# Optimization experiments

Hardware: AMD Instinct MI355X
Metric: run time of the kernel (lower is better)

Reference implementation:

```python
import jax, jax.numpy as jnp
import numpy as np

N = 20000
E = 640000
H, C = 4, 64
L = 3
B = 16
EPS = 1e-5


def setup_inputs() -> dict:
    key = jax.random.key(0)
    ks = jax.random.split(key, 12)
    x = jax.random.normal(ks[0], (N, 256), dtype=jnp.float32)
    edge_index = jax.random.randint(ks[1], (2, E), 0, N, dtype=jnp.int64)
    batch = jnp.sort(jax.random.randint(ks[2], (N,), 0, B, dtype=jnp.int64))
    s = 0.05
    return {
        "x": x,
        "edge_index": edge_index,
        "batch": batch,
        "Wl": jax.random.normal(ks[3], (L, 256, H * C), dtype=jnp.float32) * s,
        "bl": jnp.zeros((L, H * C), dtype=jnp.float32),
        "Wr": jax.random.normal(ks[4], (L, 256, H * C), dtype=jnp.float32) * s,
        "br": jnp.zeros((L, H * C), dtype=jnp.float32),
        "att": jax.random.normal(ks[5], (L, H, C), dtype=jnp.float32) * s,
        "conv_bias": jnp.zeros((L, H * C), dtype=jnp.float32),
        "prelu_a": jnp.full((L,), 0.25, dtype=jnp.float32),
        "norm_w": jnp.ones((H * C,), dtype=jnp.float32),
        "norm_b": jnp.zeros((H * C,), dtype=jnp.float32),
        "norm_alpha": jnp.ones((H * C,), dtype=jnp.float32),
        "fc_W": jax.random.normal(ks[6], (H * C, 128), dtype=jnp.float32) * s,
        "fc_b": jnp.zeros((128,), dtype=jnp.float32),
    }


def graph_norm(h, w, b, alpha):
    # GraphNorm with batch=None: all rows form one segment (as in source forward)
    mean = jnp.mean(h, axis=0, keepdims=True)
    shifted = h - alpha * mean
    var = jnp.mean(shifted * shifted, axis=0, keepdims=True)
    return w * shifted / jnp.sqrt(var + EPS) + b


def gatv2_layer(h, src, dst, Wl, bl, Wr, br, att, bias):
    xl = (h @ Wl + bl).reshape(N, H, C)  # source transform
    xr = (h @ Wr + br).reshape(N, H, C)  # target transform
    m = jax.nn.leaky_relu(xl[src] + xr[dst], negative_slope=0.2)  # [Etot,H,C]
    e = jnp.einsum("ehc,hc->eh", m, att)  # [Etot,H]
    emax = jax.ops.segment_max(e, dst, num_segments=N)  # self-loops guarantee coverage
    ex = jnp.exp(e - emax[dst])
    denom = jax.ops.segment_sum(ex, dst, num_segments=N)
    alpha = ex / denom[dst]
    out = jax.ops.segment_sum(alpha[:, :, None] * xl[src], dst, num_segments=N)
    return out.reshape(N, H * C) + bias


def reference(x, edge_index, batch, Wl, bl, Wr, br, att, conv_bias, prelu_a,
              norm_w, norm_b, norm_alpha, fc_W, fc_b):
    loop = jnp.arange(N, dtype=edge_index.dtype)
    src = jnp.concatenate([edge_index[0], loop])  # add self-loops (PyG default)
    dst = jnp.concatenate([edge_index[1], loop])
    h = x
    for l in range(L):
        h = gatv2_layer(h, src, dst, Wl[l], bl[l], Wr[l], br[l], att[l], conv_bias[l])
        h = graph_norm(h, norm_w, norm_b, norm_alpha)
        h = jnp.where(h >= 0, h, prelu_a[l] * h)  # PReLU; dropout is identity in eval
    pooled = jax.ops.segment_sum(h, batch, num_segments=B)  # global_add_pool
    pooled = graph_norm(pooled, norm_w, norm_b, norm_alpha)  # shared norm reused after pool
    return pooled @ fc_W + fc_b
```

## Files before the change

kernel.cpp:

```cpp
#include <hip/hip_runtime.h>
#include <math.h>

#define N_NODES 20000
#define N_EDGES 640000
#define ETOT (N_EDGES + N_NODES)
#define HC 256
#define NLAYER 3
#define NBATCH 16
#define GEPS 1e-5f
#define NSLOT 64

typedef unsigned short u16;
typedef unsigned int u32;
typedef __attribute__((ext_vector_type(8))) short short8;
typedef __attribute__((ext_vector_type(4))) float floatx4;

__device__ __forceinline__ u16 f2bf(float f) {
    u32 u = __float_as_uint(f);
    u32 r = (u + 0x7FFFu + ((u >> 16) & 1u)) >> 16;
    return (u16)r;
}

__device__ __forceinline__ float4 bf2f4(uint2 u) {
    float4 r;
    r.x = __uint_as_float(u.x << 16);
    r.y = __uint_as_float(u.x & 0xFFFF0000u);
    r.z = __uint_as_float(u.y << 16);
    r.w = __uint_as_float(u.y & 0xFFFF0000u);
    return r;
}

__device__ __forceinline__ float dpp_red16(float x) {
    x += __int_as_float(__builtin_amdgcn_update_dpp(0, __float_as_int(x), 0xB1, 0xF, 0xF, true));
    x += __int_as_float(__builtin_amdgcn_update_dpp(0, __float_as_int(x), 0x4E, 0xF, 0xF, true));
    x += __int_as_float(__builtin_amdgcn_update_dpp(0, __float_as_int(x), 0x141, 0xF, 0xF, true));
    x += __int_as_float(__builtin_amdgcn_update_dpp(0, __float_as_int(x), 0x140, 0xF, 0xF, true));
    return x;
}


__global__ __launch_bounds__(256) void prep(const float* __restrict__ x, u16* __restrict__ xbf,
                                            const float* __restrict__ Wl, const float* __restrict__ Wr,
                                            u16* __restrict__ WT, uint4* __restrict__ zbase, int zq) {
    int b = blockIdx.x, tid = threadIdx.x;
    if (b < 1000) {
        for (int i = b * 256 + tid; i < 640000; i += 256000) {
            const float4* x4 = (const float4*)x + (size_t)i * 2;
            float4 a = x4[0], c = x4[1];
            u16 o[8] = {f2bf(a.x), f2bf(a.y), f2bf(a.z), f2bf(a.w),
                        f2bf(c.x), f2bf(c.y), f2bf(c.z), f2bf(c.w)};
            ((uint4*)xbf)[i] = *(const uint4*)o;
        }
    } else if (b < 1384) {
        __shared__ float T[32][33];
        int bi = b - 1000;
        int kb = bi & 7, nbk = (bi >> 3) & 15, l = bi >> 7;
        int n0 = nbk * 32, k0 = kb * 32;
        const float* W = ((n0 < 256) ? Wl : Wr) + (size_t)l * 65536;
        int nn = n0 & 255;
        int tx = tid & 31, ty = tid >> 5;
        #pragma unroll
        for (int i = 0; i < 4; ++i)
            T[ty + i * 8][tx] = W[(size_t)(k0 + ty + i * 8) * 256 + nn + tx];
        __syncthreads();
        u16* outw = WT + (size_t)l * 512 * 256;
        #pragma unroll
        for (int i = 0; i < 4; ++i)
            outw[(size_t)(n0 + ty + i * 8) * 256 + k0 + tx] = f2bf(T[tx][ty + i * 8]);
    } else {
        uint4 z = make_uint4(0, 0, 0, 0);
        for (int i = (b - 1384) * 256 + tid; i < zq; i += 120 * 256) zbase[i] = z;
    }
}


__global__ void count_deg(const int* __restrict__ dst, int* __restrict__ deg) {
    int e = blockIdx.x * 256 + threadIdx.x;
    if (e < N_EDGES) atomicAdd(&deg[dst[e]], 1);
}

__global__ __launch_bounds__(1024) void scan_excl(int* __restrict__ data, int* __restrict__ cursor) {
    __shared__ int wsum[16];
    __shared__ int carry_s;
    int tid = threadIdx.x, lane = tid & 63, wid = tid >> 6;
    if (tid == 0) carry_s = 0;
    __syncthreads();
    for (int base = 0; base < N_NODES; base += 1024) {
        int i = base + tid;
        int v = (i < N_NODES) ? (data[i] + 1) : 0;
        int x = v;
        #pragma unroll
        for (int off = 1; off < 64; off <<= 1) {
            int t = __shfl_up(x, off);
            if (lane >= off) x += t;
        }
        if (lane == 63) wsum[wid] = x;
        __syncthreads();
        int carry = carry_s;
        __syncthreads();
        if (tid == 0) {
            int run = 0;
            #pragma unroll
            for (int w2 = 0; w2 < 16; ++w2) { int t = wsum[w2]; wsum[w2] = run; run += t; }
            carry_s = carry + run;
        }
        __syncthreads();
        int excl = carry + wsum[wid] + x - v;
        if (i < N_NODES) { data[i] = excl; cursor[i] = excl; }
        __syncthreads();
    }
    if (tid == 0) data[N_NODES] = carry_s;
}

__global__ void scatter_edges(const int* __restrict__ src, const int* __restrict__ dst,
                              int* __restrict__ cursor, int* __restrict__ col) {
    int t = blockIdx.x * 256 + threadIdx.x;
    if (t < N_NODES) {
        int p = atomicAdd(&cursor[t], 1);
        col[p] = t;
    } else if (t < N_NODES + N_EDGES) {
        int e = t - N_NODES;
        int p = atomicAdd(&cursor[dst[e]], 1);
        col[p] = src[e];
    }
}


__global__ __launch_bounds__(256) void gemm_mfma(
    const u16* __restrict__ Asrc, const float* __restrict__ slots_prev,
    const float* __restrict__ nw, const float* __restrict__ nb, const float* __restrict__ na,
    const float* __restrict__ pa, int prelu_idx, int use_norm,
    const u16* __restrict__ WT,
    const float* __restrict__ b0, const float* __restrict__ b1,
    u16* __restrict__ xlb, u16* __restrict__ xrb) {
    __shared__ u16 As[128][40];
    __shared__ u16 Bs[128][40];
    __shared__ float wcL[256], bbL[256];
    int row0 = blockIdx.x * 128;
    int nstrip = blockIdx.y;
    int ncol0 = nstrip * 128;
    const float* bias = (nstrip < 2) ? b0 : b1;
    u16* outp = (nstrip < 2) ? xlb : xrb;
    int c0 = (nstrip & 1) * 128;

    int tid = threadIdx.x;
    float ap = 0.f;
    if (use_norm) {
        int c = tid;
        float sum = 0.f, sq = 0.f;
        for (int s = 0; s < NSLOT; ++s) {
            sum += slots_prev[s * 512 + c];
            sq += slots_prev[s * 512 + 256 + c];
        }
        const float invn = 1.f / (float)N_NODES;
        float mean = sum * invn, Eh2 = sq * invn;
        float a = na[c];
        float var = Eh2 - (2.f * a - a * a) * mean * mean;
        float wc = nw[c] * rsqrtf(var + GEPS);
        wcL[c] = wc;
        bbL[c] = nb[c] - a * mean * wc;
        ap = pa[prelu_idx];
        __syncthreads();
    }

    int wave = tid >> 6, lane = tid & 63;
    int wm = (wave & 1) * 64, wn = (wave >> 1) * 64;
    int quad = lane >> 4, l16 = lane & 15;

    floatx4 acc[4][4] = {};

    int sr = tid >> 1;
    int sh = (tid & 1) * 16;

    for (int k0 = 0; k0 < 256; k0 += 32) {
        int gr = row0 + sr;
        uint4 av0 = make_uint4(0, 0, 0, 0), av1 = make_uint4(0, 0, 0, 0);
        if (gr < N_NODES) {
            const u16* p = Asrc + (size_t)gr * 256 + k0 + sh;
            av0 = *(const uint4*)p;
            av1 = *(const uint4*)(p + 8);
        }
        if (use_norm) {
            int kb2 = k0 + sh;
            u16 tmp[16];
            *(uint4*)tmp = av0;
            *(uint4*)(tmp + 8) = av1;
            u16 outv[16];
            #pragma unroll
            for (int j = 0; j < 16; ++j) {
                float vv = __uint_as_float(((u32)tmp[j]) << 16);
                float t2 = vv * wcL[kb2 + j] + bbL[kb2 + j];
                t2 = fmaxf(t2, ap * t2);
                outv[j] = f2bf(t2);
            }
            av0 = *(const uint4*)outv;
            av1 = *(const uint4*)(outv + 8);
        }
        const u16* q = WT + (size_t)(ncol0 + sr) * 256 + k0 + sh;
        uint4 bw0 = *(const uint4*)q;
        uint4 bw1 = *(const uint4*)(q + 8);
        *(uint4*)&As[sr][sh] = av0;
        *(uint4*)&As[sr][sh + 8] = av1;
        *(uint4*)&Bs[sr][sh] = bw0;
        *(uint4*)&Bs[sr][sh + 8] = bw1;
        __syncthreads();

        short8 af[4], bfr[4];
        #pragma unroll
        for (int mi = 0; mi < 4; ++mi)
            af[mi] = *(const short8*)&As[wm + mi * 16 + l16][quad * 8];
        #pragma unroll
        for (int ni = 0; ni < 4; ++ni)
            bfr[ni] = *(const short8*)&Bs[wn + ni * 16 + l16][quad * 8];
        #pragma unroll
        for (int mi = 0; mi < 4; ++mi)
            #pragma unroll
            for (int ni = 0; ni < 4; ++ni)
                acc[mi][ni] = __builtin_amdgcn_mfma_f32_16x16x32_bf16(af[mi], bfr[ni], acc[mi][ni], 0, 0, 0);
        __syncthreads();
    }

    #pragma unroll
    for (int ni = 0; ni < 4; ++ni) {
        int col = c0 + wn + ni * 16 + l16;
        float bv = bias[col];
        #pragma unroll
        for (int mi = 0; mi < 4; ++mi) {
            int gr = row0 + wm + mi * 16 + quad * 4;
            #pragma unroll
            for (int r = 0; r < 4; ++r) {
                if (gr + r < N_NODES)
                    outp[(size_t)(gr + r) * 256 + col] = f2bf(acc[mi][ni][r] + bv);
            }
        }
    }
}


__global__ __launch_bounds__(1024) void gat_agg(
    const u16* __restrict__ xlb, const u16* __restrict__ xrb,
    const int* __restrict__ rowptr, const int* __restrict__ col,
    const float* __restrict__ att_l, const float* __restrict__ bias_l,
    u16* __restrict__ hB, float* __restrict__ slot) {
    __shared__ float sred[16][520];
    int wid = threadIdx.x >> 6, lane = threadIdx.x & 63;
    int node = blockIdx.x * 16 + wid;
    const uint2* xl2 = (const uint2*)xlb;
    float4 attv = ((const float4*)att_l)[lane];
    float4 xrv = bf2f4(((const uint2*)xrb)[(size_t)node * 64 + lane]);
    int beg = rowptr[node], end = rowptr[node + 1];

    float denom = 0.f;
    float4 acc = make_float4(0.f, 0.f, 0.f, 0.f);

    int j = beg;
    for (; j + 8 <= end; j += 8) {
        int s[8];
        uint2 raw[8];
        float4 a[8];
        float p[8];
        #pragma unroll
        for (int u = 0; u < 8; ++u) s[u] = col[j + u];
        #pragma unroll
        for (int u = 0; u < 8; ++u) raw[u] = xl2[(size_t)s[u] * 64 + lane];
        #pragma unroll
        for (int u = 0; u < 8; ++u) {
            a[u] = bf2f4(raw[u]);
            float vx = a[u].x + xrv.x, vy = a[u].y + xrv.y;
            float vz = a[u].z + xrv.z, vw = a[u].w + xrv.w;
            vx = fmaxf(vx, 0.2f * vx);
            vy = fmaxf(vy, 0.2f * vy);
            vz = fmaxf(vz, 0.2f * vz);
            vw = fmaxf(vw, 0.2f * vw);
            p[u] = vx * attv.x + vy * attv.y + vz * attv.z + vw * attv.w;
        }
        #pragma unroll
        for (int u = 0; u < 8; ++u) p[u] = dpp_red16(p[u]);
        #pragma unroll
        for (int u = 0; u < 8; ++u) {
            float w = __expf(p[u]);
            denom += w;
            acc.x += w * a[u].x; acc.y += w * a[u].y;
            acc.z += w * a[u].z; acc.w += w * a[u].w;
        }
    }
    for (; j < end; ++j) {
        int s = col[j];
        float4 a = bf2f4(xl2[(size_t)s * 64 + lane]);
        float vx = a.x + xrv.x, vy = a.y + xrv.y;
        float vz = a.z + xrv.z, vw = a.w + xrv.w;
        vx = fmaxf(vx, 0.2f * vx);
        vy = fmaxf(vy, 0.2f * vy);
        vz = fmaxf(vz, 0.2f * vz);
        vw = fmaxf(vw, 0.2f * vw);
        float p = vx * attv.x + vy * attv.y + vz * attv.z + vw * attv.w;
        p = dpp_red16(p);
        float w = __expf(p);
        denom += w;
        acc.x += w * a.x; acc.y += w * a.y; acc.z += w * a.z; acc.w += w * a.w;
    }

    float inv = 1.f / denom;
    float4 b4 = ((const float4*)bias_l)[lane];
    float4 o;
    o.x = acc.x * inv + b4.x; o.y = acc.y * inv + b4.y;
    o.z = acc.z * inv + b4.z; o.w = acc.w * inv + b4.w;
    u16 ob[4] = {f2bf(o.x), f2bf(o.y), f2bf(o.z), f2bf(o.w)};
    ((uint2*)hB)[(size_t)node * 64 + lane] = *(const uint2*)ob;

    int cb2 = lane * 4;
    sred[wid][cb2 + 0] = o.x; sred[wid][cb2 + 1] = o.y;
    sred[wid][cb2 + 2] = o.z; sred[wid][cb2 + 3] = o.w;
    sred[wid][256 + cb2 + 0] = o.x * o.x; sred[wid][256 + cb2 + 1] = o.y * o.y;
    sred[wid][256 + cb2 + 2] = o.z * o.z; sred[wid][256 + cb2 + 3] = o.w * o.w;
    __syncthreads();
    int t = threadIdx.x;
    if (t < 512) {
        float s = 0.f;
        #pragma unroll
        for (int w = 0; w < 16; ++w) s += sred[w][t];
        atomicAdd(&slot[(blockIdx.x & (NSLOT - 1)) * 512 + t], s);
    }
}


__global__ __launch_bounds__(256) void pool_kernel(const u16* __restrict__ hB,
                                                   const int* __restrict__ batch,
                                                   const float* __restrict__ slots2,
                                                   const float* __restrict__ nw, const float* __restrict__ nb,
                                                   const float* __restrict__ na, const float* __restrict__ pa,
                                                   float* __restrict__ pooled) {
    __shared__ float accs[NBATCH][256];
    int c = threadIdx.x;
    float sum = 0.f, sq = 0.f;
    for (int s = 0; s < NSLOT; ++s) {
        sum += slots2[s * 512 + c];
        sq += slots2[s * 512 + 256 + c];
    }
    const float invn = 1.f / (float)N_NODES;
    float mean = sum * invn, Eh2 = sq * invn;
    float a = na[c];
    float var = Eh2 - (2.f * a - a * a) * mean * mean;
    float wc = nw[c] * rsqrtf(var + GEPS);
    float bb = nb[c] - a * mean * wc;
    float ap = pa[2];

    #pragma unroll
    for (int b = 0; b < NBATCH; ++b) accs[b][c] = 0.f;
    int r0 = blockIdx.x * 100;
    int r1 = min(N_NODES, r0 + 100);
    for (int i = r0; i < r1; ++i) {
        float v = __uint_as_float(((u32)hB[(size_t)i * 256 + c]) << 16);
        v = v * wc + bb;
        v = fmaxf(v, ap * v);
        accs[batch[i]][c] += v;
    }
    int bmin = batch[r0], bmax = batch[r1 - 1];
    for (int b = bmin; b <= bmax; ++b) atomicAdd(&pooled[b * 256 + c], accs[b][c]);
}


__global__ __launch_bounds__(256) void poolnorm_fc(const float* __restrict__ pooled,
                                                   const float* __restrict__ nw, const float* __restrict__ nb,
                                                   const float* __restrict__ na,
                                                   const float* __restrict__ fcW, const float* __restrict__ fcb,
                                                   float* __restrict__ out) {
    __shared__ float pn[NBATCH][256];
    int c = threadIdx.x;
    float mean = 0.f, sq = 0.f;
    #pragma unroll
    for (int i = 0; i < NBATCH; ++i) {
        float v = pooled[i * 256 + c];
        mean += v; sq += v * v;
    }
    mean *= (1.f / NBATCH); sq *= (1.f / NBATCH);
    float a = na[c];
    float var = sq - (2.f * a - a * a) * mean * mean;
    float wc = nw[c] * rsqrtf(var + GEPS);
    float bb = nb[c] - a * mean * wc;
    #pragma unroll
    for (int i = 0; i < NBATCH; ++i)
        pn[i][c] = pooled[i * 256 + c] * wc + bb;
    __syncthreads();
    int o = c & 127, bset = c >> 7;
    for (int b = bset; b < NBATCH; b += 2) {
        float s = fcb[o];
        for (int k = 0; k < 256; ++k) s += pn[b][k] * fcW[k * 128 + o];
        out[b * 128 + o] = s;
    }
}


extern "C" void kernel_launch(void* const* d_in, const int* in_sizes, int n_in,
                              void* d_out, int out_size, void* d_ws, size_t ws_size,
                              hipStream_t stream) {
    const float* x    = (const float*)d_in[0];
    const int*   ei   = (const int*)d_in[1];
    const int*   batch= (const int*)d_in[2];
    const float* Wl   = (const float*)d_in[3];
    const float* bl   = (const float*)d_in[4];
    const float* Wr   = (const float*)d_in[5];
    const float* br   = (const float*)d_in[6];
    const float* att  = (const float*)d_in[7];
    const float* cb   = (const float*)d_in[8];
    const float* pa   = (const float*)d_in[9];
    const float* nw   = (const float*)d_in[10];
    const float* nb   = (const float*)d_in[11];
    const float* na   = (const float*)d_in[12];
    const float* fcW  = (const float*)d_in[13];
    const float* fcb  = (const float*)d_in[14];
    float* out = (float*)d_out;

    char* ws = (char*)d_ws;
    size_t off = 0;
    auto carve = [&](size_t bytes) -> void* {
        void* p = (void*)(ws + off);
        off += (bytes + 255) & ~(size_t)255;
        return p;
    };
    size_t z0 = off;
    int*   rowptr = (int*)carve((N_NODES + 1) * sizeof(int));
    float* slots  = (float*)carve((size_t)NLAYER * NSLOT * 512 * sizeof(float));
    float* pooled = (float*)carve(NBATCH * HC * sizeof(float));
    size_t z1 = off;
    int*   cursor = (int*)carve(N_NODES * sizeof(int));
    int*   colidx = (int*)carve((size_t)ETOT * sizeof(int));
    u16*   xlb    = (u16*)carve((size_t)N_NODES * HC * sizeof(u16));
    u16*   xrb    = (u16*)carve((size_t)N_NODES * HC * sizeof(u16));
    u16*   hB     = (u16*)carve((size_t)N_NODES * HC * sizeof(u16));
    u16*   xbf    = (u16*)carve((size_t)N_NODES * HC * sizeof(u16));
    u16*   WT     = (u16*)carve((size_t)NLAYER * 512 * 256 * sizeof(u16));

    int zq = (int)((z1 - z0) / 16);
    const int* srcp = ei;
    const int* dstp = ei + N_EDGES;

    prep<<<1504, 256, 0, stream>>>(x, xbf, Wl, Wr, WT, (uint4*)(ws + z0), zq);
    count_deg<<<(N_EDGES + 255) / 256, 256, 0, stream>>>(dstp, rowptr);
    scan_excl<<<1, 1024, 0, stream>>>(rowptr, cursor);
    scatter_edges<<<(ETOT + 255) / 256, 256, 0, stream>>>(srcp, dstp, cursor, colidx);

    for (int l = 0; l < NLAYER; ++l) {
        const u16* Asrc = (l == 0) ? xbf : hB;
        const float* slots_prev = slots + (size_t)((l > 0) ? (l - 1) : 0) * NSLOT * 512;
        gemm_mfma<<<dim3(157, 4), 256, 0, stream>>>(Asrc, slots_prev, nw, nb, na, pa,
                                                    (l > 0) ? (l - 1) : 0, (l > 0) ? 1 : 0,
                                                    WT + (size_t)l * 512 * 256,
                                                    bl + l * 256, br + l * 256, xlb, xrb);
        gat_agg<<<1250, 1024, 0, stream>>>(xlb, xrb, rowptr, colidx, att + l * 256, cb + l * 256,
                                           hB, slots + (size_t)l * NSLOT * 512);
    }
    pool_kernel<<<200, 256, 0, stream>>>(hB, batch, slots + (size_t)2 * NSLOT * 512,
                                         nw, nb, na, pa, pooled);
    poolnorm_fc<<<1, 256, 0, stream>>>(pooled, nw, nb, na, fcW, fcb, out);
}
```

Before: 533.8 us.

## Parallelize scan, shrink aggregation blocks, vectorize norm loads, split final FC

The degree scan now runs in one pass: each of 1024 threads handles 20 contiguous nodes, replacing the 20-iteration loop with repeated barriers. The aggregation kernel moves from 1024-thread to 256-thread blocks, four nodes per block, which gives finer scheduling but four times as many atomic adds into the stats slots. The norm weights in the GEMM prologue are loaded as float4 vectors. The single-block pool-norm and FC step is split into a norm kernel and a 16-block FC kernel, which adds one launch but spreads the FC work across more compute units.

```diff
diff --git a/kernel.cpp b/kernel.cpp
--- a/kernel.cpp
+++ b/kernel.cpp
@@ -81,35 +81,39 @@
 
 __global__ __launch_bounds__(1024) void scan_excl(int* __restrict__ data, int* __restrict__ cursor) {
     __shared__ int wsum[16];
-    __shared__ int carry_s;
-    int tid = threadIdx.x, lane = tid & 63, wid = tid >> 6;
-    if (tid == 0) carry_s = 0;
+    int t = threadIdx.x, lane = t & 63, wid = t >> 6;
+    int i0 = t * 20;
+    int d[20];
+    int tot = 0;
+    #pragma unroll
+    for (int j = 0; j < 20; ++j) {
+        int i = i0 + j;
+        int v = (i < N_NODES) ? (data[i] + 1) : 0;
+        d[j] = v;
+        tot += v;
+    }
+    int x = tot;
+    #pragma unroll
+    for (int off = 1; off < 64; off <<= 1) {
+        int tmp = __shfl_up(x, off);
+        if (lane >= off) x += tmp;
+    }
+    if (lane == 63) wsum[wid] = x;
     __syncthreads();
-    for (int base = 0; base < N_NODES; base += 1024) {
-        int i = base + tid;
-        int v = (i < N_NODES) ? (data[i] + 1) : 0;
-        int x = v;
-        #pragma unroll
-        for (int off = 1; off < 64; off <<= 1) {
-            int t = __shfl_up(x, off);
-            if (lane >= off) x += t;
-        }
-        if (lane == 63) wsum[wid] = x;
-        __syncthreads();
-        int carry = carry_s;
-        __syncthreads();
-        if (tid == 0) {
-            int run = 0;
-            #pragma unroll
-            for (int w2 = 0; w2 < 16; ++w2) { int t = wsum[w2]; wsum[w2] = run; run += t; }
-            carry_s = carry + run;
-        }
-        __syncthreads();
-        int excl = carry + wsum[wid] + x - v;
-        if (i < N_NODES) { data[i] = excl; cursor[i] = excl; }
-        __syncthreads();
-    }
-    if (tid == 0) data[N_NODES] = carry_s;
+    if (t == 0) {
+        int run = 0;
+        #pragma unroll
+        for (int w = 0; w < 16; ++w) { int tv = wsum[w]; wsum[w] = run; run += tv; }
+    }
+    __syncthreads();
+    int run = wsum[wid] + x - tot;
+    #pragma unroll
+    for (int j = 0; j < 20; ++j) {
+        int i = i0 + j;
+        if (i < N_NODES) { data[i] = run; cursor[i] = run; }
+        run += d[j];
+    }
+    if (t == 0) data[N_NODES] = ETOT;
 }
 
 __global__ void scatter_edges(const int* __restrict__ src, const int* __restrict__ dst,
@@ -185,11 +189,19 @@
             u16 tmp[16];
             *(uint4*)tmp = av0;
             *(uint4*)(tmp + 8) = av1;
+            float4 wv0 = *(const float4*)&wcL[kb2], wv1 = *(const float4*)&wcL[kb2 + 4];
+            float4 wv2 = *(const float4*)&wcL[kb2 + 8], wv3 = *(const float4*)&wcL[kb2 + 12];
+            float4 bv0 = *(const float4*)&bbL[kb2], bv1 = *(const float4*)&bbL[kb2 + 4];
+            float4 bv2 = *(const float4*)&bbL[kb2 + 8], bv3 = *(const float4*)&bbL[kb2 + 12];
+            float wvf[16] = {wv0.x, wv0.y, wv0.z, wv0.w, wv1.x, wv1.y, wv1.z, wv1.w,
+                             wv2.x, wv2.y, wv2.z, wv2.w, wv3.x, wv3.y, wv3.z, wv3.w};
+            float bvf[16] = {bv0.x, bv0.y, bv0.z, bv0.w, bv1.x, bv1.y, bv1.z, bv1.w,
+                             bv2.x, bv2.y, bv2.z, bv2.w, bv3.x, bv3.y, bv3.z, bv3.w};
             u16 outv[16];
             #pragma unroll
             for (int j = 0; j < 16; ++j) {
                 float vv = __uint_as_float(((u32)tmp[j]) << 16);
-                float t2 = vv * wcL[kb2 + j] + bbL[kb2 + j];
+                float t2 = vv * wvf[j] + bvf[j];
                 t2 = fmaxf(t2, ap * t2);
                 outv[j] = f2bf(t2);
             }
@@ -237,14 +249,14 @@
 }
 
 
-__global__ __launch_bounds__(1024) void gat_agg(
+__global__ __launch_bounds__(256) void gat_agg(
     const u16* __restrict__ xlb, const u16* __restrict__ xrb,
     const int* __restrict__ rowptr, const int* __restrict__ col,
     const float* __restrict__ att_l, const float* __restrict__ bias_l,
     u16* __restrict__ hB, float* __restrict__ slot) {
-    __shared__ float sred[16][520];
+    __shared__ float sred[4][520];
     int wid = threadIdx.x >> 6, lane = threadIdx.x & 63;
-    int node = blockIdx.x * 16 + wid;
+    int node = blockIdx.x * 4 + wid;
     const uint2* xl2 = (const uint2*)xlb;
     float4 attv = ((const float4*)att_l)[lane];
     float4 xrv = bf2f4(((const uint2*)xrb)[(size_t)node * 64 + lane]);
@@ -315,11 +327,11 @@
     sred[wid][256 + cb2 + 2] = o.z * o.z; sred[wid][256 + cb2 + 3] = o.w * o.w;
     __syncthreads();
     int t = threadIdx.x;
-    if (t < 512) {
-        float s = 0.f;
-        #pragma unroll
-        for (int w = 0; w < 16; ++w) s += sred[w][t];
-        atomicAdd(&slot[(blockIdx.x & (NSLOT - 1)) * 512 + t], s);
+    #pragma unroll
+    for (int h = 0; h < 2; ++h) {
+        int idx = t + h * 256;
+        float s = sred[0][idx] + sred[1][idx] + sred[2][idx] + sred[3][idx];
+        atomicAdd(&slot[(blockIdx.x & (NSLOT - 1)) * 512 + idx], s);
     }
 }
 
@@ -360,12 +372,10 @@
 }
 
 
-__global__ __launch_bounds__(256) void poolnorm_fc(const float* __restrict__ pooled,
-                                                   const float* __restrict__ nw, const float* __restrict__ nb,
-                                                   const float* __restrict__ na,
-                                                   const float* __restrict__ fcW, const float* __restrict__ fcb,
-                                                   float* __restrict__ out) {
-    __shared__ float pn[NBATCH][256];
+__global__ __launch_bounds__(256) void pool_norm(const float* __restrict__ pooled,
+                                                 const float* __restrict__ nw, const float* __restrict__ nb,
+                                                 const float* __restrict__ na,
+                                                 float* __restrict__ pn) {
     int c = threadIdx.x;
     float mean = 0.f, sq = 0.f;
     #pragma unroll
@@ -380,14 +390,28 @@
     float bb = nb[c] - a * mean * wc;
     #pragma unroll
     for (int i = 0; i < NBATCH; ++i)
-        pn[i][c] = pooled[i * 256 + c] * wc + bb;
+        pn[i * 256 + c] = pooled[i * 256 + c] * wc + bb;
+}
+
+
+__global__ __launch_bounds__(256) void fc_kernel(const float* __restrict__ pn,
+                                                 const float* __restrict__ fcW, const float* __restrict__ fcb,
+                                                 float* __restrict__ out) {
+    __shared__ float pnl[256];
+    __shared__ float part[128];
+    int b = blockIdx.x;
+    int t = threadIdx.x;
+    pnl[t] = pn[b * 256 + t];
     __syncthreads();
-    int o = c & 127, bset = c >> 7;
-    for (int b = bset; b < NBATCH; b += 2) {
-        float s = fcb[o];
-        for (int k = 0; k < 256; ++k) s += pn[b][k] * fcW[k * 128 + o];
-        out[b * 128 + o] = s;
-    }
+    int o = t & 127, half = t >> 7;
+    float s = 0.f;
+    int kbase = half * 128;
+    #pragma unroll 8
+    for (int k = 0; k < 128; ++k)
+        s += pnl[kbase + k] * fcW[(kbase + k) * 128 + o];
+    if (half == 1) part[o] = s;
+    __syncthreads();
+    if (half == 0) out[b * 128 + o] = s + part[o] + fcb[o];
 }
 
 
@@ -430,6 +454,7 @@
     u16*   hB     = (u16*)carve((size_t)N_NODES * HC * sizeof(u16));
     u16*   xbf    = (u16*)carve((size_t)N_NODES * HC * sizeof(u16));
     u16*   WT     = (u16*)carve((size_t)NLAYER * 512 * 256 * sizeof(u16));
+    float* pn     = (float*)carve(NBATCH * HC * sizeof(float));
 
     int zq = (int)((z1 - z0) / 16);
     const int* srcp = ei;
@@ -447,10 +472,11 @@
                                                     (l > 0) ? (l - 1) : 0, (l > 0) ? 1 : 0,
                                                     WT + (size_t)l * 512 * 256,
                                                     bl + l * 256, br + l * 256, xlb, xrb);
-        gat_agg<<<1250, 1024, 0, stream>>>(xlb, xrb, rowptr, colidx, att + l * 256, cb + l * 256,
-                                           hB, slots + (size_t)l * NSLOT * 512);
+        gat_agg<<<5000, 256, 0, stream>>>(xlb, xrb, rowptr, colidx, att + l * 256, cb + l * 256,
+                                          hB, slots + (size_t)l * NSLOT * 512);
     }
     pool_kernel<<<200, 256, 0, stream>>>(hB, batch, slots + (size_t)2 * NSLOT * 512,
                                          nw, nb, na, pa, pooled);
-    poolnorm_fc<<<1, 256, 0, stream>>>(pooled, nw, nb, na, fcW, fcb, out);
-}
+    pool_norm<<<1, 256, 0, stream>>>(pooled, nw, nb, na, pn);
+    fc_kernel<<<NBATCH, 256, 0, stream>>>(pn, fcW, fcb, out);
+}
```

New measurement: 488.5 us. 1.09x faster.
